# Optimization experiments

Measured on AMD Instinct MI355X. Metric: run time of the kernel, lower is better.

The kernel has to match this reference:

```python
import jax, jax.numpy as jnp
import numpy as np

B, T, D = 32, 4096, 256          # batch, seq_len, input_dim
H = 64                           # CausalEventModel hidden (hard-coded in __init__)
A = D + 3                        # anchor_dim = input_dim + 3
K_DIM = 256                      # lift output dim (k_dim)
D_MODEL = 1024                   # topology_proj output dim
MAX_PROXY = 16                   # max_proxy_points


def setup_inputs() -> dict:
    key = jax.random.key(0)
    ks = jax.random.split(key, 6)
    def w(k, shape, fan):
        return jax.random.normal(k, shape, jnp.float32) * (1.0 / np.sqrt(fan))
    return {
        "x": jax.random.normal(ks[0], (B, T, D), jnp.float32),
        # CausalEventModel: 2-layer MLP scorer -> event_scores [B,T]
        "W1": w(ks[1], (D, H), D), "b1": jnp.zeros((H,), jnp.float32),
        "W2": w(ks[2], (H, 1), H), "b2": jnp.zeros((1,), jnp.float32),
        # NormalizedLift: (v-mu)/sigma then tanh(Linear(anchor_dim->k_dim))
        "Wl": w(ks[3], (A, K_DIM), A), "bl": jnp.zeros((K_DIM,), jnp.float32),
        "mu": jnp.zeros((A,), jnp.float32), "sigma": jnp.ones((A,), jnp.float32),
        # topology_proj: Linear(k_dim -> d_model)
        "Wp": w(ks[4], (K_DIM, D_MODEL), K_DIM), "bp": jnp.zeros((D_MODEL,), jnp.float32),
    }


def reference(x, W1, b1, W2, b2, Wl, bl, mu, sigma, Wp, bp):
    # --- event model: per-timestep saliency scores [B, T] ---
    h = jax.nn.relu(jnp.einsum("btd,dh->bth", x, W1) + b1)
    event_scores = (jnp.einsum("bth,ho->bto", h, W2) + b2)[..., 0]
    sal = jax.nn.sigmoid(event_scores)                     # saliency_scores [B, T]
    Bn, Tn = sal.shape

    # --- uniform index selection + one-hot scatter ---
    k_eff = min(Tn, MAX_PROXY)
    idx = jnp.linspace(0.0, Tn - 1, k_eff).astype(jnp.int32)   # [K_eff]
    y_star = jnp.zeros((Bn, Tn), x.dtype).at[:, idx].set(1.0)  # scatter_ ones

    # --- dense anchor vectors: concat(x, saliency, time, cum-saliency) [B,T,D+3] ---
    t_norm = jnp.broadcast_to((jnp.arange(Tn, dtype=x.dtype) / Tn)[None, :, None],
                              (Bn, Tn, 1))
    cum = (jnp.cumsum(sal, axis=1) / Tn)[..., None]
    anchors = jnp.concatenate([x, sal[..., None], t_norm, cum], axis=-1)

    # --- topology projection: L2-normalize onto unit sphere ---
    v = anchors / (jnp.linalg.norm(anchors, axis=-1, keepdims=True) + 1e-6)

    # --- NormalizedLift over the FULL dense sequence (the wasted compute) ---
    z = (v - mu) / sigma
    lifted = jnp.tanh(jnp.einsum("bta,ak->btk", z, Wl) + bl)   # [B, T, K_DIM]

    # --- gather K_eff positions, then final projection ---
    cloud = lifted[:, idx, :]                                  # [B, K_eff, K_DIM]
    tokens = jnp.einsum("bkc,cm->bkm", cloud, Wp) + bp         # [B, K_eff, D_MODEL]
    return tokens, y_star
```

## Files before the change

### kernel.cpp

```cpp
#include <hip/hip_runtime.h>
#include <hip/hip_bf16.h>
#include <math.h>

#define B_ 32
#define T_ 4096
#define D_ 256
#define H_ 64
#define A_ 259
#define K_ 256
#define M_ 1024
#define P_ 16
#define STEP_ 273

typedef __attribute__((ext_vector_type(8))) short bf16x8;
typedef __attribute__((ext_vector_type(4))) float f32x4;

__device__ __forceinline__ short f32_to_bf16_rne(float f) {
    unsigned u = __builtin_bit_cast(unsigned, f);
    unsigned r = (u + 0x7fffu + ((u >> 16) & 1u)) >> 16;
    return (short)r;
}

__global__ __launch_bounds__(256) void k1_sal(
    const float* __restrict__ x, const float* __restrict__ W1,
    const float* __restrict__ b1, const float* __restrict__ W2,
    const float* __restrict__ b2, float* __restrict__ sal)
{
    __shared__ short w1f[8][4][64 * 8];
    const int tid = threadIdx.x;

    #pragma unroll
    for (int i = 0; i < 8; ++i) {
        const int e = tid + i * 256;
        const int lane = e & 63;
        const int ktnt = e >> 6;
        const int kt = ktnt >> 2, nt = ktnt & 3;
        const int n  = nt * 16 + (lane & 15);
        const int k0 = kt * 32 + (lane >> 4) * 8;
        bf16x8 v;
        #pragma unroll
        for (int j = 0; j < 8; ++j)
            v[j] = f32_to_bf16_rne(W1[(size_t)(k0 + j) * H_ + n]);
        *(bf16x8*)&w1f[kt][nt][lane * 8] = v;
    }
    __syncthreads();

    const int wave = tid >> 6, lane = tid & 63;
    const int m = lane & 15, q = lane >> 4;
    const int rowbase = blockIdx.x * 64 + wave * 16;
    const float* xrow = x + (size_t)(rowbase + m) * D_ + q * 8;

    f32x4 acc[4] = {{0,0,0,0},{0,0,0,0},{0,0,0,0},{0,0,0,0}};

    #pragma unroll
    for (int kt = 0; kt < 8; ++kt) {
        const float4 p0 = *(const float4*)(xrow + kt * 32);
        const float4 p1 = *(const float4*)(xrow + kt * 32 + 4);
        bf16x8 a;
        a[0] = f32_to_bf16_rne(p0.x); a[1] = f32_to_bf16_rne(p0.y);
        a[2] = f32_to_bf16_rne(p0.z); a[3] = f32_to_bf16_rne(p0.w);
        a[4] = f32_to_bf16_rne(p1.x); a[5] = f32_to_bf16_rne(p1.y);
        a[6] = f32_to_bf16_rne(p1.z); a[7] = f32_to_bf16_rne(p1.w);
        #pragma unroll
        for (int nt = 0; nt < 4; ++nt) {
            const bf16x8 bfr = *(const bf16x8*)&w1f[kt][nt][lane * 8];
            acc[nt] = __builtin_amdgcn_mfma_f32_16x16x32_bf16(a, bfr, acc[nt], 0, 0, 0);
        }
    }

    float part[4];
    #pragma unroll
    for (int reg = 0; reg < 4; ++reg) {
        float s = 0.f;
        #pragma unroll
        for (int nt = 0; nt < 4; ++nt) {
            const int n = nt * 16 + m;
            const float hv = acc[nt][reg] + b1[n];
            s = fmaf(fmaxf(hv, 0.f), W2[n], s);
        }
        part[reg] = s;
    }
    #pragma unroll
    for (int off = 1; off < 16; off <<= 1) {
        #pragma unroll
        for (int reg = 0; reg < 4; ++reg)
            part[reg] += __shfl_xor(part[reg], off, 64);
    }
    const int r3 = m & 3;
    const float myv = (r3 == 0) ? part[0] : (r3 == 1) ? part[1]
                    : (r3 == 2) ? part[2] : part[3];
    if (m < 4) {
        const float score = myv + b2[0];
        sal[rowbase + q * 4 + m] = 1.f / (1.f + __expf(-score));
    }
}

__global__ __launch_bounds__(256) void k2_scan(
    const float* __restrict__ sal, float* __restrict__ cumsel,
    float* __restrict__ ystar)
{
    __shared__ float vals[T_];
    __shared__ float tsum[256];
    const int b = blockIdx.x;
    const int t = threadIdx.x;

    const float4* sp = (const float4*)(sal + (size_t)b * T_);
    float v[16];
    #pragma unroll
    for (int q = 0; q < 4; ++q) {
        float4 f = sp[t * 4 + q];
        v[q*4+0] = f.x; v[q*4+1] = f.y; v[q*4+2] = f.z; v[q*4+3] = f.w;
    }
    float run = 0.f;
    #pragma unroll
    for (int k = 0; k < 16; ++k) { run += v[k]; v[k] = run; }

    tsum[t] = run;
    __syncthreads();
    float val = run;
    for (int off = 1; off < 256; off <<= 1) {
        float add = (t >= off) ? tsum[t - off] : 0.f;
        __syncthreads();
        val += add;
        tsum[t] = val;
        __syncthreads();
    }
    const float offset = val - run;
    #pragma unroll
    for (int k = 0; k < 16; ++k) vals[t * 16 + k] = offset + v[k];

    float ys[16];
    #pragma unroll
    for (int k = 0; k < 16; ++k)
        ys[k] = (((t * 16 + k) % STEP_) == 0) ? 1.f : 0.f;
    float4* yo = (float4*)(ystar + (size_t)b * T_ + t * 16);
    #pragma unroll
    for (int q = 0; q < 4; ++q)
        yo[q] = make_float4(ys[q*4+0], ys[q*4+1], ys[q*4+2], ys[q*4+3]);

    __syncthreads();
    if (t < P_) cumsel[b * P_ + t] = vals[STEP_ * t] * (1.0f / (float)T_);
}

__global__ __launch_bounds__(256) void k3a_lift(
    const float* __restrict__ x, const float* __restrict__ sal,
    const float* __restrict__ cumsel, const float* __restrict__ Wl,
    const float* __restrict__ bl, const float* __restrict__ mu,
    const float* __restrict__ sigma, float* __restrict__ lift)
{
    __shared__ float z[4][260];
    __shared__ float part[4 * 4 * 256];
    const int tid = threadIdx.x;
    const int wave = tid >> 6, lane = tid & 63;

    {
        const int r = wave;
        const int s = blockIdx.x * 4 + r;
        const int b = s >> 4, i = s & 15;
        const int pos = STEP_ * i;
        const float* xrow = x + ((size_t)b * T_ + pos) * D_;
        const float4 xv = *(const float4*)(xrow + 4 * lane);
        const float sv = sal[b * T_ + pos];
        const float tn = (float)pos * (1.0f / (float)T_);
        const float cv = cumsel[b * P_ + i];

        float p = xv.x*xv.x + xv.y*xv.y + xv.z*xv.z + xv.w*xv.w;
        #pragma unroll
        for (int off = 32; off > 0; off >>= 1) p += __shfl_xor(p, off, 64);
        const float ss = p + sv * sv + tn * tn + cv * cv;
        const float inv = 1.0f / (sqrtf(ss) + 1e-6f);

        const float4 muv = *(const float4*)(mu + 4 * lane);
        const float4 sgv = *(const float4*)(sigma + 4 * lane);
        z[r][4*lane+0] = (xv.x * inv - muv.x) / sgv.x;
        z[r][4*lane+1] = (xv.y * inv - muv.y) / sgv.y;
        z[r][4*lane+2] = (xv.z * inv - muv.z) / sgv.z;
        z[r][4*lane+3] = (xv.w * inv - muv.w) / sgv.w;
        if (lane < 3) {
            const float e = (lane == 0) ? sv : (lane == 1) ? tn : cv;
            z[r][256 + lane] = (e * inv - mu[256 + lane]) / sigma[256 + lane];
        }
    }
    __syncthreads();

    const int a0 = wave * 65;
    const int a1 = (wave == 3) ? A_ : a0 + 65;
    f32x4 acc[4] = {{0,0,0,0},{0,0,0,0},{0,0,0,0},{0,0,0,0}};
    const float4* Wl4 = (const float4*)Wl;

    #pragma unroll 4
    for (int a = a0; a < a1; ++a) {
        const float4 wv = Wl4[a * 64 + lane];
        #pragma unroll
        for (int r = 0; r < 4; ++r) {
            const float zv = z[r][a];
            acc[r][0] = fmaf(zv, wv.x, acc[r][0]);
            acc[r][1] = fmaf(zv, wv.y, acc[r][1]);
            acc[r][2] = fmaf(zv, wv.z, acc[r][2]);
            acc[r][3] = fmaf(zv, wv.w, acc[r][3]);
        }
    }
    {
        f32x4* p4 = (f32x4*)part;
        #pragma unroll
        for (int r = 0; r < 4; ++r)
            p4[(wave * 4 + r) * 64 + lane] = acc[r];
    }
    __syncthreads();

    const int r = tid >> 6;
    const size_t base = (size_t)blockIdx.x * 4 * K_;
    #pragma unroll
    for (int j = 0; j < 4; ++j) {
        const int k = lane + 64 * j;
        float val = bl[k];
        #pragma unroll
        for (int w = 0; w < 4; ++w)
            val += part[(w * 4 + r) * 256 + k];
        lift[base + r * K_ + k] = tanhf(val);
    }
}

__global__ __launch_bounds__(256) void k3b_tok(
    const float* __restrict__ lift, const float* __restrict__ Wp,
    const float* __restrict__ bp, float* __restrict__ tokens)
{
    __shared__ float ls[8 * K_];
    __shared__ float part[4 * 8 * 256];
    const int tid = threadIdx.x;
    const int wave = tid >> 6, lane = tid & 63;
    const int mt = blockIdx.x & 3;
    const int rh = (blockIdx.x >> 2) & 1;
    const int b  = blockIdx.x >> 3;
    const int s0 = b * P_ + rh * 8;
    const int m0 = mt * 256;

    const float4* lg = (const float4*)(lift + (size_t)s0 * K_);
    float4* lsl = (float4*)ls;
    lsl[tid] = lg[tid];
    lsl[tid + 256] = lg[tid + 256];
    __syncthreads();

    f32x4 acc[8] = {{0,0,0,0},{0,0,0,0},{0,0,0,0},{0,0,0,0},
                    {0,0,0,0},{0,0,0,0},{0,0,0,0},{0,0,0,0}};
    const float4* Wp4 = (const float4*)(Wp + m0);

    #pragma unroll 2
    for (int c4 = 0; c4 < 16; ++c4) {
        const int c = wave * 64 + c4 * 4;
        float4 lsv[8];
        #pragma unroll
        for (int r = 0; r < 8; ++r)
            lsv[r] = *(const float4*)&ls[r * K_ + c];
        #pragma unroll
        for (int cc = 0; cc < 4; ++cc) {
            const float4 wv = Wp4[(size_t)(c + cc) * 256 + lane];
            #pragma unroll
            for (int r = 0; r < 8; ++r) {
                const float lv = (cc == 0) ? lsv[r].x : (cc == 1) ? lsv[r].y
                               : (cc == 2) ? lsv[r].z : lsv[r].w;
                acc[r][0] = fmaf(lv, wv.x, acc[r][0]);
                acc[r][1] = fmaf(lv, wv.y, acc[r][1]);
                acc[r][2] = fmaf(lv, wv.z, acc[r][2]);
                acc[r][3] = fmaf(lv, wv.w, acc[r][3]);
            }
        }
    }
    {
        f32x4* p4 = (f32x4*)part;
        #pragma unroll
        for (int r = 0; r < 8; ++r)
            p4[(wave * 8 + r) * 64 + lane] = acc[r];
    }
    __syncthreads();

    const float bv = bp[m0 + tid];
    #pragma unroll
    for (int r = 0; r < 8; ++r) {
        float val = bv;
        #pragma unroll
        for (int w = 0; w < 4; ++w)
            val += part[(w * 8 + r) * 256 + tid];
        tokens[(size_t)(s0 + r) * M_ + m0 + tid] = val;
    }
}

extern "C" void kernel_launch(void* const* d_in, const int* in_sizes, int n_in,
                              void* d_out, int out_size, void* d_ws, size_t ws_size,
                              hipStream_t stream)
{
    (void)in_sizes; (void)n_in; (void)out_size; (void)ws_size;
    const float* x  = (const float*)d_in[0];
    const float* W1 = (const float*)d_in[1];
    const float* b1 = (const float*)d_in[2];
    const float* W2 = (const float*)d_in[3];
    const float* b2 = (const float*)d_in[4];
    const float* Wl = (const float*)d_in[5];
    const float* bl = (const float*)d_in[6];
    const float* mu = (const float*)d_in[7];
    const float* sg = (const float*)d_in[8];
    const float* Wp = (const float*)d_in[9];
    const float* bp = (const float*)d_in[10];

    float* out    = (float*)d_out;
    float* tokens = out;
    float* ystar  = out + (size_t)B_ * P_ * M_;

    float* ws     = (float*)d_ws;
    float* sal    = ws;
    float* cumsel = ws + (size_t)B_ * T_;
    float* lift   = cumsel + B_ * P_;

    k1_sal<<<dim3((B_ * T_) / 64), dim3(256), 0, stream>>>(x, W1, b1, W2, b2, sal);
    k2_scan<<<dim3(B_), dim3(256), 0, stream>>>(sal, cumsel, ystar);
    k3a_lift<<<dim3((B_ * P_) / 4), dim3(256), 0, stream>>>(x, sal, cumsel, Wl, bl, mu, sg, lift);
    k3b_tok<<<dim3(B_ * 2 * 4), dim3(256), 0, stream>>>(lift, Wp, bp, tokens);
}
```

Before: 247.7 us.

## Process two row groups per block in saliency kernel and parallelize cumsum selection

The saliency kernel now handles 128 rows per block across two iterations. Each iteration loads all x fragments up front before converting them, and the kernel declares an occupancy hint of 4 blocks per CU. This amortizes the W1 staging into shared memory and exposes more memory-level parallelism. The scan kernel replaces the 32-block full prefix scan with 512 blocks, each reducing a prefix sum up to one selected index, and ystar is written with one element per thread. This trades redundant reads of the saliency array for far more parallelism and no serial scan.

```diff
diff --git a/kernel.cpp b/kernel.cpp
--- a/kernel.cpp
+++ b/kernel.cpp
@@ -21,7 +21,7 @@
     return (short)r;
 }
 
-__global__ __launch_bounds__(256) void k1_sal(
+__global__ __launch_bounds__(256, 4) void k1_sal(
     const float* __restrict__ x, const float* __restrict__ W1,
     const float* __restrict__ b1, const float* __restrict__ W2,
     const float* __restrict__ b2, float* __restrict__ sal)
@@ -47,51 +47,61 @@
 
     const int wave = tid >> 6, lane = tid & 63;
     const int m = lane & 15, q = lane >> 4;
-    const int rowbase = blockIdx.x * 64 + wave * 16;
-    const float* xrow = x + (size_t)(rowbase + m) * D_ + q * 8;
-
-    f32x4 acc[4] = {{0,0,0,0},{0,0,0,0},{0,0,0,0},{0,0,0,0}};
-
-    #pragma unroll
-    for (int kt = 0; kt < 8; ++kt) {
-        const float4 p0 = *(const float4*)(xrow + kt * 32);
-        const float4 p1 = *(const float4*)(xrow + kt * 32 + 4);
-        bf16x8 a;
-        a[0] = f32_to_bf16_rne(p0.x); a[1] = f32_to_bf16_rne(p0.y);
-        a[2] = f32_to_bf16_rne(p0.z); a[3] = f32_to_bf16_rne(p0.w);
-        a[4] = f32_to_bf16_rne(p1.x); a[5] = f32_to_bf16_rne(p1.y);
-        a[6] = f32_to_bf16_rne(p1.z); a[7] = f32_to_bf16_rne(p1.w);
-        #pragma unroll
-        for (int nt = 0; nt < 4; ++nt) {
-            const bf16x8 bfr = *(const bf16x8*)&w1f[kt][nt][lane * 8];
-            acc[nt] = __builtin_amdgcn_mfma_f32_16x16x32_bf16(a, bfr, acc[nt], 0, 0, 0);
-        }
-    }
-
-    float part[4];
-    #pragma unroll
-    for (int reg = 0; reg < 4; ++reg) {
-        float s = 0.f;
-        #pragma unroll
-        for (int nt = 0; nt < 4; ++nt) {
-            const int n = nt * 16 + m;
-            const float hv = acc[nt][reg] + b1[n];
-            s = fmaf(fmaxf(hv, 0.f), W2[n], s);
-        }
-        part[reg] = s;
-    }
-    #pragma unroll
-    for (int off = 1; off < 16; off <<= 1) {
-        #pragma unroll
-        for (int reg = 0; reg < 4; ++reg)
-            part[reg] += __shfl_xor(part[reg], off, 64);
-    }
-    const int r3 = m & 3;
-    const float myv = (r3 == 0) ? part[0] : (r3 == 1) ? part[1]
-                    : (r3 == 2) ? part[2] : part[3];
-    if (m < 4) {
-        const float score = myv + b2[0];
-        sal[rowbase + q * 4 + m] = 1.f / (1.f + __expf(-score));
+    const int row0 = blockIdx.x * 128;
+
+    #pragma unroll 1
+    for (int g = 0; g < 2; ++g) {
+        const int rowbase = row0 + g * 64 + wave * 16;
+        const float* xrow = x + (size_t)(rowbase + m) * D_ + q * 8;
+
+        float4 xb[16];
+        #pragma unroll
+        for (int kt = 0; kt < 8; ++kt) {
+            xb[2 * kt]     = *(const float4*)(xrow + kt * 32);
+            xb[2 * kt + 1] = *(const float4*)(xrow + kt * 32 + 4);
+        }
+
+        f32x4 acc[4] = {{0,0,0,0},{0,0,0,0},{0,0,0,0},{0,0,0,0}};
+        #pragma unroll
+        for (int kt = 0; kt < 8; ++kt) {
+            const float4 p0 = xb[2 * kt], p1 = xb[2 * kt + 1];
+            bf16x8 a;
+            a[0] = f32_to_bf16_rne(p0.x); a[1] = f32_to_bf16_rne(p0.y);
+            a[2] = f32_to_bf16_rne(p0.z); a[3] = f32_to_bf16_rne(p0.w);
+            a[4] = f32_to_bf16_rne(p1.x); a[5] = f32_to_bf16_rne(p1.y);
+            a[6] = f32_to_bf16_rne(p1.z); a[7] = f32_to_bf16_rne(p1.w);
+            #pragma unroll
+            for (int nt = 0; nt < 4; ++nt) {
+                const bf16x8 bfr = *(const bf16x8*)&w1f[kt][nt][lane * 8];
+                acc[nt] = __builtin_amdgcn_mfma_f32_16x16x32_bf16(a, bfr, acc[nt], 0, 0, 0);
+            }
+        }
+
+        float part[4];
+        #pragma unroll
+        for (int reg = 0; reg < 4; ++reg) {
+            float s = 0.f;
+            #pragma unroll
+            for (int nt = 0; nt < 4; ++nt) {
+                const int n = nt * 16 + m;
+                const float hv = acc[nt][reg] + b1[n];
+                s = fmaf(fmaxf(hv, 0.f), W2[n], s);
+            }
+            part[reg] = s;
+        }
+        #pragma unroll
+        for (int off = 1; off < 16; off <<= 1) {
+            #pragma unroll
+            for (int reg = 0; reg < 4; ++reg)
+                part[reg] += __shfl_xor(part[reg], off, 64);
+        }
+        const int r3 = m & 3;
+        const float myv = (r3 == 0) ? part[0] : (r3 == 1) ? part[1]
+                        : (r3 == 2) ? part[2] : part[3];
+        if (m < 4) {
+            const float score = myv + b2[0];
+            sal[rowbase + q * 4 + m] = 1.f / (1.f + __expf(-score));
+        }
     }
 }
 
@@ -99,47 +109,27 @@
     const float* __restrict__ sal, float* __restrict__ cumsel,
     float* __restrict__ ystar)
 {
-    __shared__ float vals[T_];
-    __shared__ float tsum[256];
-    const int b = blockIdx.x;
-    const int t = threadIdx.x;
-
-    const float4* sp = (const float4*)(sal + (size_t)b * T_);
-    float v[16];
+    const int tid = threadIdx.x;
+
+    {
+        const int g = blockIdx.x * 256 + tid;
+        const int ty = g & (T_ - 1);
+        ystar[g] = ((ty % STEP_) == 0) ? 1.f : 0.f;
+    }
+
+    const int b = blockIdx.x >> 4, i = blockIdx.x & 15;
+    const int len = STEP_ * i + 1;
+    const float* sp = sal + (size_t)b * T_;
+    float s = 0.f;
+    for (int t = tid; t < len; t += 256) s += sp[t];
+
     #pragma unroll
-    for (int q = 0; q < 4; ++q) {
-        float4 f = sp[t * 4 + q];
-        v[q*4+0] = f.x; v[q*4+1] = f.y; v[q*4+2] = f.z; v[q*4+3] = f.w;
-    }
-    float run = 0.f;
-    #pragma unroll
-    for (int k = 0; k < 16; ++k) { run += v[k]; v[k] = run; }
-
-    tsum[t] = run;
-    __syncthreads();
-    float val = run;
-    for (int off = 1; off < 256; off <<= 1) {
-        float add = (t >= off) ? tsum[t - off] : 0.f;
-        __syncthreads();
-        val += add;
-        tsum[t] = val;
-        __syncthreads();
-    }
-    const float offset = val - run;
-    #pragma unroll
-    for (int k = 0; k < 16; ++k) vals[t * 16 + k] = offset + v[k];
-
-    float ys[16];
-    #pragma unroll
-    for (int k = 0; k < 16; ++k)
-        ys[k] = (((t * 16 + k) % STEP_) == 0) ? 1.f : 0.f;
-    float4* yo = (float4*)(ystar + (size_t)b * T_ + t * 16);
-    #pragma unroll
-    for (int q = 0; q < 4; ++q)
-        yo[q] = make_float4(ys[q*4+0], ys[q*4+1], ys[q*4+2], ys[q*4+3]);
-
-    __syncthreads();
-    if (t < P_) cumsel[b * P_ + t] = vals[STEP_ * t] * (1.0f / (float)T_);
+    for (int off = 32; off > 0; off >>= 1) s += __shfl_xor(s, off, 64);
+    __shared__ float red[4];
+    if ((tid & 63) == 0) red[tid >> 6] = s;
+    __syncthreads();
+    if (tid == 0)
+        cumsel[b * P_ + i] = (red[0] + red[1] + red[2] + red[3]) * (1.0f / (float)T_);
 }
 
 __global__ __launch_bounds__(256) void k3a_lift(
@@ -311,8 +301,8 @@
     float* cumsel = ws + (size_t)B_ * T_;
     float* lift   = cumsel + B_ * P_;
 
-    k1_sal<<<dim3((B_ * T_) / 64), dim3(256), 0, stream>>>(x, W1, b1, W2, b2, sal);
-    k2_scan<<<dim3(B_), dim3(256), 0, stream>>>(sal, cumsel, ystar);
+    k1_sal<<<dim3((B_ * T_) / 128), dim3(256), 0, stream>>>(x, W1, b1, W2, b2, sal);
+    k2_scan<<<dim3(B_ * P_), dim3(256), 0, stream>>>(sal, cumsel, ystar);
     k3a_lift<<<dim3((B_ * P_) / 4), dim3(256), 0, stream>>>(x, sal, cumsel, Wl, bl, mu, sg, lift);
     k3b_tok<<<dim3(B_ * 2 * 4), dim3(256), 0, stream>>>(lift, Wp, bp, tokens);
 }
```

After: 269.4 us. +8.8%, slower.
